# Kernel tuning notes

Hardware: AMD Instinct MI355X
Metric: run time of the kernel (lower is better)

## Reference

```python
import jax, jax.numpy as jnp
import numpy as np

B, M, N, R, FIN, D, H = 16, 512, 512, 8, 4, 256, 4
DH = D // H
LGAT = 2
TF_RATE, THRESH = 0.9, 2.0
GAT_W, ORG_W, DET_W = 0.5, 0.5, 0.5


def setup_inputs() -> dict:
    key = jax.random.key(0)
    ks = jax.random.split(key, 16)
    g = lambda k, shp, fan: jax.random.normal(k, shp, jnp.float32) / np.sqrt(fan)
    inp = {
        'tracks': jax.random.normal(ks[0], (B, M, R, FIN), jnp.float32),
        'detections': jax.random.normal(ks[1], (B, N, FIN), jnp.float32),
        'tracklet_marks': jax.random.randint(ks[2], (B,), M // 2, M + 1, jnp.int32),
        'detection_marks': jax.random.randint(ks[3], (B,), N // 2, N + 1, jnp.int32),
        'feat_W1': g(ks[4], (FIN, D), FIN),
        'feat_b1': jnp.zeros((D,), jnp.float32),
        'feat_W2': g(ks[5], (D, D), D),
        'feat_b2': jnp.zeros((D,), jnp.float32),
        'enc_Wqkv': g(ks[6], (D, 3 * D), D),
        'enc_Wo': g(ks[7], (D, D), D),
        'enc_ff1': g(ks[8], (D, 4 * D), D),
        'enc_ff2': g(ks[9], (4 * D, D), 4 * D),
        'gat_W': g(ks[10], (LGAT, D, D), D),
        'gat_a': g(ks[11], (LGAT, 2, H, DH), DH),
        'det_gat_W': g(ks[12], (LGAT, D, D), D),
        'det_gat_a': g(ks[13], (LGAT, 2, H, DH), DH),
        'cls_Wq': g(ks[14], (2, D, D), D),
        'cls_Wk': g(ks[15], (2, D, D), D),
    }
    return inp


def _ln(x):
    m = jnp.mean(x, -1, keepdims=True)
    v = jnp.var(x, -1, keepdims=True)
    return (x - m) * jax.lax.rsqrt(v + 1e-5)


def _feat(x, W1, b1, W2, b2):
    return jax.nn.elu(x @ W1 + b1) @ W2 + b2


def _encoder(x, Wqkv, Wo, ff1, ff2):
    # x: [T, R, D] -> one pre-LN transformer layer over the rewind axis
    T = x.shape[0]
    h = _ln(x)
    qkv = (h @ Wqkv).reshape(T, R, 3, H, DH)
    q, k, v = qkv[:, :, 0], qkv[:, :, 1], qkv[:, :, 2]
    att = jax.nn.softmax(jnp.einsum('trhd,tshd->thrs', q, k) / np.sqrt(DH), axis=-1)
    o = jnp.einsum('thrs,tshd->trhd', att, v).reshape(T, R, D) @ Wo
    x = x + o
    return x + jax.nn.relu(_ln(x) @ ff1) @ ff2


def _gat(x, adj, W, a):
    # x: [B, Nn, D]; adj: [B, Nn, Nn] bool; a: [2, H, DH]
    b, nn_, _ = x.shape
    h = (x @ W).reshape(b, nn_, H, DH)
    src = jnp.einsum('bnhd,hd->bnh', h, a[0])
    dst = jnp.einsum('bnhd,hd->bnh', h, a[1])
    e = jax.nn.leaky_relu(src[:, :, None, :] + dst[:, None, :, :], 0.2)  # [B,Nn,Nn,H]
    e = jnp.where(adj[..., None], e, -1e9)
    alpha = jax.nn.softmax(e, axis=2)
    out = jnp.einsum('bijh,bjhd->bihd', alpha, h).reshape(b, nn_, D)
    return jax.nn.elu(out)


def _scores(x, adj_f, Wq, Wk):
    s = jax.nn.sigmoid(jnp.einsum('bid,bjd->bij', x @ Wq, x @ Wk) / np.sqrt(D))
    return s * adj_f


def _forward(tracks, detections, tracklet_marks, detection_marks,
             feat_W1, feat_b1, feat_W2, feat_b2,
             enc_Wqkv, enc_Wo, enc_ff1, enc_ff2,
             gat_W, gat_a, det_gat_W, det_gat_a, cls_Wq, cls_Wk):
    tr_emb = _feat(tracks, feat_W1, feat_b1, feat_W2, feat_b2)      # [B,M,R,D]
    det_emb = _feat(detections, feat_W1, feat_b1, feat_W2, feat_b2)  # [B,N,D]

    enc = _encoder(tr_emb.reshape(B * M, R, D), enc_Wqkv, enc_Wo, enc_ff1, enc_ff2)
    enc = enc.reshape(B, M, R, D)
    predicted = tr_emb[:, :, 0, :] + TF_RATE * enc[:, :, 0, :]       # [B,M,D]

    tmask = jnp.arange(M)[None, :] < tracklet_marks[:, None]
    dmask = jnp.arange(N)[None, :] < detection_marks[:, None]

    pos = jnp.concatenate([tracks[:, :, 0, :2], detections[:, :, :2]], axis=1)  # [B,M+N,2]
    vmask = jnp.concatenate([tmask, dmask], axis=1)
    dist = jnp.linalg.norm(pos[:, :, None, :] - pos[:, None, :, :], axis=-1)
    adj = (dist < THRESH) & vmask[:, :, None] & vmask[:, None, :]
    adj_f = adj.astype(jnp.float32)

    feat0 = jnp.concatenate([predicted, det_emb], axis=1)  # [B,M+N,D]
    x = feat0
    for l in range(LGAT):
        x = GAT_W * _gat(x, adj, gat_W[l], gat_a[l]) + ORG_W * feat0
    scores = _scores(x, adj_f, cls_Wq[0], cls_Wk[0])       # [B,M+N,M+N]
    asso_results = scores[:, :M, M:]                        # track->det block

    pd = detections[:, :, :2]
    dist_d = jnp.linalg.norm(pd[:, :, None, :] - pd[:, None, :, :], axis=-1)
    adj_d = (dist_d < THRESH) & dmask[:, :, None] & dmask[:, None, :]
    adj_d_f = adj_d.astype(jnp.float32)

    xd = det_emb
    for l in range(LGAT):
        xd = DET_W * _gat(xd, adj_d, det_gat_W[l], det_gat_a[l]) + ORG_W * det_emb
    det_scores = _scores(xd, adj_d_f, cls_Wq[1], cls_Wk[1])
    det_scores = det_scores * (1.0 - jnp.eye(N, dtype=jnp.float32))  # zero_diag

    return scores, det_scores, asso_results


def reference(tracks, detections, tracklet_marks, detection_marks,
              feat_W1, feat_b1, feat_W2, feat_b2,
              enc_Wqkv, enc_Wo, enc_ff1, enc_ff2,
              gat_W, gat_a, det_gat_W, det_gat_a, cls_Wq, cls_Wk):
    return _forward(tracks, detections, tracklet_marks, detection_marks,
                    feat_W1, feat_b1, feat_W2, feat_b2,
                    enc_Wqkv, enc_Wo, enc_ff1, enc_ff2,
                    gat_W, gat_a, det_gat_W, det_gat_a, cls_Wq, cls_Wk)
```

## Files before the change

kernel.cpp:

```cpp
#include <hip/hip_runtime.h>
#include <math.h>


typedef __bf16 bf16;
typedef __bf16 bf16x8 __attribute__((ext_vector_type(8)));
typedef __bf16 bf16x4 __attribute__((ext_vector_type(4)));
typedef float f32x4 __attribute__((ext_vector_type(4)));

__device__ __forceinline__ float bf2f(bf16 x) { return (float)x; }
__device__ __forceinline__ bf16 f2bf(float x) { return (bf16)x; }

__device__ __forceinline__ bool node_adj(float4 a, float4 c) {
    float dx = a.x - c.x, dy = a.y - c.y;
    return (sqrtf(dx * dx + dy * dy) + a.z + c.z) < 2.0f;
}

struct PrepEnt { const float* src; long dofs; int R; int C; int tstart; };
struct PrepTab { PrepEnt e[13]; };

__global__ __launch_bounds__(256) void k_prep(PrepTab tab, bf16* __restrict__ dst)
{
    __shared__ float tile[32][33];
    const int tid = blockIdx.x;
    int k = 0;
    #pragma unroll
    for (int q = 1; q < 13; ++q) if (tid >= tab.e[q].tstart) k = q;
    PrepEnt E = tab.e[k];
    const int local = tid - E.tstart;
    const int cT = E.C >> 5;
    const int tr = local / cT, tc = local - tr * cT;
    const int r0 = tr << 5, c0 = tc << 5;
    const int t = threadIdx.x;
    {
        int r = t >> 3, cq = (t & 7) * 4;
        *(float4*)&tile[r][cq] = *(const float4*)(E.src + (long)(r0 + r) * E.C + c0 + cq);
    }
    __syncthreads();
    {
        int c = t >> 3, rq = (t & 7) * 4;
        bf16x4 o;
        o[0] = f2bf(tile[rq + 0][c]); o[1] = f2bf(tile[rq + 1][c]);
        o[2] = f2bf(tile[rq + 2][c]); o[3] = f2bf(tile[rq + 3][c]);
        *(bf16x4*)(dst + E.dofs + (long)(c0 + c) * E.R + r0 + rq) = o;
    }
}

__device__ __forceinline__ void gemm_bt(const bf16* __restrict__ A, int lda,
                                        const bf16* __restrict__ BT, int ldb,
                                        int K, f32x4 acc[4])
{
    __shared__ bf16 As[64][40];
    __shared__ bf16 Bs[64][40];
    const int t = threadIdx.x;
    const int m0 = blockIdx.y * 64;
    const int n0 = blockIdx.x * 64;
    const int lane = t & 63, wv = t >> 6, lr = lane & 15, kq = lane >> 4;
    const int arow = t >> 2, acol = (t & 3) * 8;
    for (int k0 = 0; k0 < K; k0 += 32) {
        __syncthreads();
        *(uint4*)&As[arow][acol] = *(const uint4*)(A + (long)(m0 + arow) * lda + k0 + acol);
        *(uint4*)&Bs[arow][acol] = *(const uint4*)(BT + (long)(n0 + arow) * ldb + k0 + acol);
        __syncthreads();
        bf16x8 af = *(const bf16x8*)&As[wv * 16 + lr][kq * 8];
        #pragma unroll
        for (int nt = 0; nt < 4; ++nt) {
            bf16x8 bfr = *(const bf16x8*)&Bs[nt * 16 + lr][kq * 8];
            acc[nt] = __builtin_amdgcn_mfma_f32_16x16x32_bf16(af, bfr, acc[nt], 0, 0, 0);
        }
    }
}

__global__ __launch_bounds__(256) void k_gemm_bf16(
    const bf16* __restrict__ A, int lda,
    const bf16* __restrict__ BT, int ldb,
    bf16* __restrict__ out, int ldo, int K, int relu)
{
    f32x4 acc[4] = {};
    gemm_bt(A, lda, BT, ldb, K, acc);
    const int lane = threadIdx.x & 63, wv = threadIdx.x >> 6;
    const int lr = lane & 15, kq = lane >> 4;
    const int m0 = blockIdx.y * 64, n0 = blockIdx.x * 64;
    #pragma unroll
    for (int nt = 0; nt < 4; ++nt) {
        int col = n0 + nt * 16 + lr;
        #pragma unroll
        for (int i = 0; i < 4; ++i) {
            int row = m0 + wv * 16 + kq * 4 + i;
            float v = acc[nt][i];
            if (relu) v = fmaxf(v, 0.f);
            out[(long)row * ldo + col] = f2bf(v);
        }
    }
}

__global__ __launch_bounds__(256) void k_gemm_addres(
    const bf16* __restrict__ A, int lda,
    const bf16* __restrict__ BT, int ldb,
    const float* __restrict__ res1, int ldr1,
    float* __restrict__ outf, int ldo, int K)
{
    f32x4 acc[4] = {};
    gemm_bt(A, lda, BT, ldb, K, acc);
    const int lane = threadIdx.x & 63, wv = threadIdx.x >> 6;
    const int lr = lane & 15, kq = lane >> 4;
    const int m0 = blockIdx.y * 64, n0 = blockIdx.x * 64;
    #pragma unroll
    for (int nt = 0; nt < 4; ++nt) {
        int col = n0 + nt * 16 + lr;
        #pragma unroll
        for (int i = 0; i < 4; ++i) {
            int row = m0 + wv * 16 + kq * 4 + i;
            outf[(long)row * ldo + col] = res1[(long)row * ldr1 + col] + acc[nt][i];
        }
    }
}

__global__ __launch_bounds__(256) void k_gemm_pred(
    const bf16* __restrict__ A, int lda,
    const bf16* __restrict__ BT, int ldb,
    const float* __restrict__ res1, const float* __restrict__ res2,
    float* __restrict__ outf, bf16* __restrict__ outb, int K)
{
    f32x4 acc[4] = {};
    gemm_bt(A, lda, BT, ldb, K, acc);
    const int lane = threadIdx.x & 63, wv = threadIdx.x >> 6;
    const int lr = lane & 15, kq = lane >> 4;
    const int m0 = blockIdx.y * 64, n0 = blockIdx.x * 64;
    #pragma unroll
    for (int nt = 0; nt < 4; ++nt) {
        int col = n0 + nt * 16 + lr;
        #pragma unroll
        for (int i = 0; i < 4; ++i) {
            int row = m0 + wv * 16 + kq * 4 + i;
            float v = res1[(long)row * 256 + col]
                    + 0.9f * (res2[(long)row * 256 + col] + acc[nt][i]);
            long drow = (long)row + ((row >> 9) << 9);
            long o = drow * 256 + col;
            outf[o] = v;
            outb[o] = f2bf(v);
        }
    }
}

__global__ __launch_bounds__(256) void k_gemm_logits(
    const bf16* __restrict__ A, long sAz,
    const bf16* __restrict__ Bm, long sBz, int K,
    float* __restrict__ out, int ldo, long sOz,
    const float4* __restrict__ nodes, int nodeOfs,
    float* __restrict__ asso, int flags)
{
    f32x4 acc[4] = {};
    const int z = blockIdx.z;
    gemm_bt(A + z * sAz, 256, Bm + z * sBz, 256, K, acc);
    const int lane = threadIdx.x & 63, wv = threadIdx.x >> 6;
    const int lr = lane & 15, kq = lane >> 4;
    const int m0 = blockIdx.y * 64, n0 = blockIdx.x * 64;
    const float4* nb = nodes + z * 1024 + nodeOfs;
    float4 nrow[4], ncol[4];
    #pragma unroll
    for (int i = 0; i < 4; ++i) nrow[i] = nb[m0 + wv * 16 + kq * 4 + i];
    #pragma unroll
    for (int nt = 0; nt < 4; ++nt) ncol[nt] = nb[n0 + nt * 16 + lr];
    float* ob = out + z * sOz;
    #pragma unroll
    for (int nt = 0; nt < 4; ++nt) {
        int col = n0 + nt * 16 + lr;
        #pragma unroll
        for (int i = 0; i < 4; ++i) {
            int row = m0 + wv * 16 + kq * 4 + i;
            bool adj = node_adj(nrow[i], ncol[nt]);
            if ((flags & 2) && row == col) adj = false;
            float v = 0.f;
            if (adj) v = 1.f / (1.f + __expf(-acc[nt][i] * 0.0625f));
            ob[(long)row * ldo + col] = v;
            if ((flags & 1) && row < 512 && col >= 512)
                asso[(long)z * 262144 + (long)row * 512 + (col - 512)] = v;
        }
    }
}

__global__ __launch_bounds__(256) void k_gemm_T(
    const bf16* __restrict__ WT, const bf16* __restrict__ X,
    bf16* __restrict__ hgT, int nN, int nLog)
{
    f32x4 acc[4] = {};
    gemm_bt(WT, 256, X, 256, 256, acc);
    const int lane = threadIdx.x & 63, wv = threadIdx.x >> 6;
    const int lr = lane & 15, kq = lane >> 4;
    const int d0 = blockIdx.y * 64, n0 = blockIdx.x * 64;
    #pragma unroll
    for (int nt = 0; nt < 4; ++nt) {
        int node = n0 + nt * 16 + lr;
        int b = node >> nLog;
        int j = node & (nN - 1);
        #pragma unroll
        for (int i = 0; i < 4; ++i) {
            int d = d0 + wv * 16 + kq * 4 + i;
            hgT[((long)(b * 256 + d) << nLog) + j] = f2bf(acc[nt][i]);
        }
    }
}

__global__ __launch_bounds__(256) void k_featgemm(
    const float* __restrict__ tracks, const float* __restrict__ dets,
    const float* __restrict__ W1, const float* __restrict__ b1,
    const bf16* __restrict__ W2T, const float* __restrict__ b2,
    bf16* __restrict__ emb_b, float* __restrict__ emb_r0_f,
    float* __restrict__ feat0_f, bf16* __restrict__ feat0_b,
    bf16* __restrict__ demb_b)
{
    __shared__ float xr[64][4];
    __shared__ float w1s[4][256];
    __shared__ float b1s[256];
    __shared__ bf16 As[64][40];
    __shared__ bf16 Bs[256][40];
    const int t = threadIdx.x;
    const int m0 = blockIdx.x * 64;
    if (t < 64) {
        int gr = m0 + t;
        const float* sp = (gr < 65536) ? (tracks + (long)gr * 4)
                                       : (dets + (long)(gr - 65536) * 4);
        *(float4*)&xr[t][0] = *(const float4*)sp;
    }
    w1s[0][t] = W1[t];       w1s[1][t] = W1[256 + t];
    w1s[2][t] = W1[512 + t]; w1s[3][t] = W1[768 + t];
    b1s[t] = b1[t];
    const int arow = t >> 2, acol = (t & 3) * 8;
    const int lane = t & 63, wv = t >> 6, lr = lane & 15, kq = lane >> 4;
    f32x4 acc[16] = {};
    __syncthreads();
    for (int k0 = 0; k0 < 256; k0 += 32) {
        __syncthreads();
        #pragma unroll
        for (int j = 0; j < 8; ++j) {
            int c = k0 + acol + j;
            float v = fmaf(xr[arow][0], w1s[0][c],
                      fmaf(xr[arow][1], w1s[1][c],
                      fmaf(xr[arow][2], w1s[2][c],
                      fmaf(xr[arow][3], w1s[3][c], b1s[c]))));
            v = v > 0.f ? v : (__expf(v) - 1.f);
            As[arow][acol + j] = f2bf(v);
        }
        #pragma unroll
        for (int rr = 0; rr < 4; ++rr) {
            int n = rr * 64 + (t >> 2);
            *(uint4*)&Bs[n][acol] = *(const uint4*)(W2T + (long)n * 256 + k0 + acol);
        }
        __syncthreads();
        bf16x8 af = *(const bf16x8*)&As[wv * 16 + lr][kq * 8];
        #pragma unroll
        for (int nt = 0; nt < 16; ++nt) {
            bf16x8 bfr = *(const bf16x8*)&Bs[nt * 16 + lr][kq * 8];
            acc[nt] = __builtin_amdgcn_mfma_f32_16x16x32_bf16(af, bfr, acc[nt], 0, 0, 0);
        }
    }
    #pragma unroll
    for (int nt = 0; nt < 16; ++nt) {
        int col = nt * 16 + lr;
        float bv = b2[col];
        #pragma unroll
        for (int i = 0; i < 4; ++i) {
            int gr = m0 + wv * 16 + kq * 4 + i;
            float v = acc[nt][i] + bv;
            emb_b[(long)gr * 256 + col] = f2bf(v);
            if (gr < 65536) {
                if ((gr & 7) == 0) emb_r0_f[(long)(gr >> 3) * 256 + col] = v;
            } else {
                int dr = gr - 65536;
                long drow = ((long)(dr >> 9) << 10) + 512 + (dr & 511);
                feat0_f[drow * 256 + col] = v;
                feat0_b[drow * 256 + col] = f2bf(v);
                demb_b[(long)dr * 256 + col] = f2bf(v);
            }
        }
    }
}

__global__ __launch_bounds__(256) void k_adjmask(
    const float4* __restrict__ nodes, unsigned long long* __restrict__ adjm,
    int nN, int nLog, int nodeOfs)
{
    const int bi = blockIdx.x;
    const int b = bi >> nLog;
    const int i = bi & (nN - 1);
    const float4* nb = nodes + b * 1024 + nodeOfs;
    const float4 ni = nb[i];
    const int t = threadIdx.x;
    const int w = t >> 6, lane = t & 63;
    const int nC = nN >> 6;
    for (int it = 0; it * 256 < nN; ++it) {
        int j = it * 256 + t;
        bool adj = node_adj(ni, nb[j]);
        unsigned long long mask = __ballot(adj);
        if (lane == 0) adjm[(long)bi * nC + it * 4 + w] = mask;
    }
}

__global__ __launch_bounds__(256) void k_ln_bf16(const bf16* __restrict__ x, bf16* __restrict__ out)
{
    const int w = threadIdx.x >> 6, l = threadIdx.x & 63;
    const long row = (long)blockIdx.x * 4 + w;
    bf16x4 xv = *(const bf16x4*)(x + row * 256 + l * 4);
    float v0 = bf2f(xv[0]), v1 = bf2f(xv[1]), v2 = bf2f(xv[2]), v3 = bf2f(xv[3]);
    float s = v0 + v1 + v2 + v3;
    #pragma unroll
    for (int o = 32; o; o >>= 1) s += __shfl_xor(s, o, 64);
    float mean = s * (1.f / 256.f);
    float d0 = v0 - mean, d1 = v1 - mean, d2 = v2 - mean, d3 = v3 - mean;
    float q = d0 * d0 + d1 * d1 + d2 * d2 + d3 * d3;
    #pragma unroll
    for (int o = 32; o; o >>= 1) q += __shfl_xor(q, o, 64);
    float rstd = rsqrtf(q * (1.f / 256.f) + 1e-5f);
    bf16x4 ov;
    ov[0] = f2bf(d0 * rstd); ov[1] = f2bf(d1 * rstd);
    ov[2] = f2bf(d2 * rstd); ov[3] = f2bf(d3 * rstd);
    *(bf16x4*)(out + row * 256 + l * 4) = ov;
}

__global__ __launch_bounds__(256) void k_ln_f32(const float* __restrict__ x, bf16* __restrict__ out)
{
    const int w = threadIdx.x >> 6, l = threadIdx.x & 63;
    const long row = (long)blockIdx.x * 4 + w;
    float4 xv = *(const float4*)(x + row * 256 + l * 4);
    float s = xv.x + xv.y + xv.z + xv.w;
    #pragma unroll
    for (int o = 32; o; o >>= 1) s += __shfl_xor(s, o, 64);
    float mean = s * (1.f / 256.f);
    float d0 = xv.x - mean, d1 = xv.y - mean, d2 = xv.z - mean, d3 = xv.w - mean;
    float q = d0 * d0 + d1 * d1 + d2 * d2 + d3 * d3;
    #pragma unroll
    for (int o = 32; o; o >>= 1) q += __shfl_xor(q, o, 64);
    float rstd = rsqrtf(q * (1.f / 256.f) + 1e-5f);
    bf16x4 ov;
    ov[0] = f2bf(d0 * rstd); ov[1] = f2bf(d1 * rstd);
    ov[2] = f2bf(d2 * rstd); ov[3] = f2bf(d3 * rstd);
    *(bf16x4*)(out + row * 256 + l * 4) = ov;
}

__global__ __launch_bounds__(256) void k_attn(
    const bf16* __restrict__ q, const bf16* __restrict__ kv,
    bf16* __restrict__ o0)
{
    const long t = blockIdx.x;
    const int h = threadIdx.x >> 6;
    const int lane = threadIdx.x & 63;
    const int s = lane >> 3;
    const int dg = lane & 7;
    const bf16* qp = q + t * 256 + h * 64 + dg * 8;
    const bf16* kp = kv + (t * 8 + s) * 512 + h * 64 + dg * 8;
    float p = 0.f;
    #pragma unroll
    for (int e = 0; e < 8; ++e) p += bf2f(qp[e]) * bf2f(kp[e]);
    p += __shfl_xor(p, 1, 64);
    p += __shfl_xor(p, 2, 64);
    p += __shfl_xor(p, 4, 64);
    float sc = p * 0.125f;
    float w[8];
    float mx = -1e30f;
    #pragma unroll
    for (int s2 = 0; s2 < 8; ++s2) { w[s2] = __shfl(sc, s2 * 8, 64); mx = fmaxf(mx, w[s2]); }
    float sum = 0.f;
    #pragma unroll
    for (int s2 = 0; s2 < 8; ++s2) { w[s2] = __expf(w[s2] - mx); sum += w[s2]; }
    float rs = 1.f / sum;
    float acc = 0.f;
    const bf16* vp = kv + (t * 8) * 512 + 256 + h * 64 + lane;
    #pragma unroll
    for (int s2 = 0; s2 < 8; ++s2) acc += w[s2] * bf2f(vp[(long)s2 * 512]);
    o0[t * 256 + h * 64 + lane] = f2bf(acc * rs);
}

__global__ __launch_bounds__(256) void k_nodes(
    const float* __restrict__ tracks, const float* __restrict__ dets,
    const int* __restrict__ tm, const int* __restrict__ dm,
    float4* __restrict__ nodes)
{
    int idx = blockIdx.x * 256 + threadIdx.x;
    int b = idx >> 10;
    int i = idx & 1023;
    float x, y;
    int valid;
    if (i < 512) {
        long o = (long)(b * 512 + i) * 32;
        x = tracks[o]; y = tracks[o + 1];
        valid = (i < tm[b]) ? 1 : 0;
    } else {
        int n = i - 512;
        long o = (long)(b * 512 + n) * 4;
        x = dets[o]; y = dets[o + 1];
        valid = (n < dm[b]) ? 1 : 0;
    }
    nodes[idx] = make_float4(x, y, valid ? 0.f : 1e9f, 0.f);
}

__global__ __launch_bounds__(256) void k_srcdst_T(
    const bf16* __restrict__ hgT, const float* __restrict__ av,
    float* __restrict__ src, float* __restrict__ dst, int nN, int nLog)
{
    __shared__ float avs[512];
    const int t = threadIdx.x;
    avs[t] = av[t]; avs[256 + t] = av[256 + t];
    __syncthreads();
    const int jl = t & 63, h = t >> 6;
    const int n = blockIdx.x * 64 + jl;
    const int b = n >> nLog, j = n & (nN - 1);
    const bf16* base = hgT + (((long)b * 256 + h * 64) << nLog) + j;
    float p0 = 0.f, p1 = 0.f;
    #pragma unroll 8
    for (int dd = 0; dd < 64; ++dd) {
        float v = bf2f(base[(long)dd << nLog]);
        p0 += v * avs[h * 64 + dd];
        p1 += v * avs[256 + h * 64 + dd];
    }
    src[(long)n * 4 + h] = p0;
    dst[(long)n * 4 + h] = p1;
}

__global__ __launch_bounds__(256) void k_maxdst(
    const float4* __restrict__ dstv, float4* __restrict__ maxd, int nN)
{
    const int b = blockIdx.x;
    const int t = threadIdx.x;
    float4 mv = make_float4(-1e30f, -1e30f, -1e30f, -1e30f);
    for (int j = t; j < nN; j += 256) {
        float4 dj = dstv[(long)b * nN + j];
        mv.x = fmaxf(mv.x, dj.x); mv.y = fmaxf(mv.y, dj.y);
        mv.z = fmaxf(mv.z, dj.z); mv.w = fmaxf(mv.w, dj.w);
    }
    __shared__ float4 red[256];
    red[t] = mv;
    __syncthreads();
    for (int off = 128; off; off >>= 1) {
        if (t < off) {
            float4 a = red[t], c = red[t + off];
            red[t] = make_float4(fmaxf(a.x, c.x), fmaxf(a.y, c.y),
                                 fmaxf(a.z, c.z), fmaxf(a.w, c.w));
        }
        __syncthreads();
    }
    if (t == 0) maxd[b] = red[0];
}

__global__ __launch_bounds__(256) void k_gatagg_mm(
    const bf16* __restrict__ hgT,
    const unsigned long long* __restrict__ adjm,
    const float4* __restrict__ srcv, const float4* __restrict__ maxd,
    const float4* __restrict__ dstv,
    const float* __restrict__ res, int resBatchStride,
    bf16* __restrict__ outb, int nN)
{
    __shared__ float dstT[4][1024];
    __shared__ unsigned int adjW[32][33];
    const int t = threadIdx.x;
    const int nblk = nN >> 5;
    const int b = blockIdx.x / nblk;
    const int i0 = (blockIdx.x - b * nblk) << 5;
    const int nC = nN >> 6;
    for (int j = t; j < nN; j += 256) {
        float4 dj = dstv[(long)b * nN + j];
        dstT[0][j] = dj.x; dstT[1][j] = dj.y; dstT[2][j] = dj.z; dstT[3][j] = dj.w;
    }
    for (int idx = t; idx < 32 * nC; idx += 256) {
        int r = idx / nC, c = idx - r * nC;
        unsigned long long v = adjm[((long)b * nN + i0 + r) * nC + c];
        adjW[r][c * 2] = (unsigned)v;
        adjW[r][c * 2 + 1] = (unsigned)(v >> 32);
    }
    __syncthreads();
    const int h = t >> 6, lane = t & 63, lr = lane & 15, kq = lane >> 4;
    const float mdh = ((const float*)(maxd + b))[h];
    float s_r[2], m_r[2], psum[2] = {0.f, 0.f};
    #pragma unroll
    for (int mt = 0; mt < 2; ++mt) {
        long idx = (long)b * nN + i0 + mt * 16 + lr;
        s_r[mt] = ((const float*)(srcv + idx))[h];
        float tmp = s_r[mt] + mdh;
        m_r[mt] = fmaxf(tmp, 0.2f * tmp);
    }
    f32x4 acc[2][4] = {};
    const bf16* hb = hgT + ((long)b * 256 + h * 64) * nN;
    for (int j0 = 0; j0 < nN; j0 += 32) {
        bf16x8 bfr[4];
        #pragma unroll
        for (int nt = 0; nt < 4; ++nt)
            bfr[nt] = *(const bf16x8*)(hb + (long)(nt * 16 + lr) * nN + j0 + kq * 8);
        #pragma unroll
        for (int mt = 0; mt < 2; ++mt) {
            unsigned byte = (adjW[mt * 16 + lr][j0 >> 5] >> (kq * 8)) & 0xffu;
            bf16x8 af;
            float ps = 0.f;
            #pragma unroll
            for (int jj = 0; jj < 8; ++jj) {
                float e = s_r[mt] + dstT[h][j0 + kq * 8 + jj];
                e = fmaxf(e, 0.2f * e);
                e = (byte & (1u << jj)) ? e : -1e9f;
                float p = __expf(e - m_r[mt]);
                af[jj] = f2bf(p);
                ps += p;
            }
            psum[mt] += ps;
            #pragma unroll
            for (int nt = 0; nt < 4; ++nt)
                acc[mt][nt] = __builtin_amdgcn_mfma_f32_16x16x32_bf16(af, bfr[nt], acc[mt][nt], 0, 0, 0);
        }
    }
    float stot[2];
    #pragma unroll
    for (int mt = 0; mt < 2; ++mt) {
        float v = psum[mt];
        v += __shfl_xor(v, 16, 64);
        v += __shfl_xor(v, 32, 64);
        stot[mt] = v;
    }
    #pragma unroll
    for (int mt = 0; mt < 2; ++mt) {
        #pragma unroll
        for (int ii = 0; ii < 4; ++ii) {
            int i = i0 + mt * 16 + kq * 4 + ii;
            long bi = (long)b * nN + i;
            float sv = __shfl(stot[mt], kq * 4 + ii, 64);
            float rs = 1.f / fmaxf(sv, 1e-30f);
            #pragma unroll
            for (int nt = 0; nt < 4; ++nt) {
                int col = h * 64 + nt * 16 + lr;
                float a = acc[mt][nt][ii] * rs;
                float e = a > 0.f ? a : expm1f(a);
                float v = 0.5f * e + 0.5f * res[(long)b * resBatchStride + (long)i * 256 + col];
                outb[bi * 256 + col] = f2bf(v);
            }
        }
    }
}

extern "C" void kernel_launch(void* const* d_in, const int* in_sizes, int n_in,
                              void* d_out, int out_size, void* d_ws, size_t ws_size,
                              hipStream_t stream)
{
    (void)in_sizes; (void)n_in; (void)out_size; (void)ws_size;
    const float* tracks = (const float*)d_in[0];
    const float* dets   = (const float*)d_in[1];
    const int*  tmarks = (const int*)d_in[2];
    const int*  dmarks = (const int*)d_in[3];
    const float* W1   = (const float*)d_in[4];
    const float* b1   = (const float*)d_in[5];
    const float* W2   = (const float*)d_in[6];
    const float* b2   = (const float*)d_in[7];
    const float* Wqkv = (const float*)d_in[8];
    const float* Wo   = (const float*)d_in[9];
    const float* eff1 = (const float*)d_in[10];
    const float* eff2 = (const float*)d_in[11];
    const float* gatW = (const float*)d_in[12];
    const float* gatA = (const float*)d_in[13];
    const float* dgatW = (const float*)d_in[14];
    const float* dgatA = (const float*)d_in[15];
    const float* clsWq = (const float*)d_in[16];
    const float* clsWk = (const float*)d_in[17];
    float* out = (float*)d_out;

    char* wsb = (char*)d_ws;
    size_t off = 0;
    auto take = [&](size_t bytes) -> char* {
        char* p = wsb + off;
        off += (bytes + 255) & ~(size_t)255;
        return p;
    };
    char* R_emb  = take(37748736);
    char* R_r0   = take(8388608);
    char* R_hln  = take(33554432);
    char* R_v    = take(33554432);
    char* R_gat  = take(25165824);
    char* R_q    = take(4194304);
    char* R_o0   = take(4194304);
    char* R_f0f  = take(16777216);
    char* R_f0b  = take(8388608);
    char* R_demb = take(4194304);
    float4* nodes = (float4*)take(262144);
    float4* src4  = (float4*)take(262144);
    float4* dst4  = (float4*)take(262144);
    float4* maxd4 = (float4*)take(256);
    unsigned long long* adjm_main = (unsigned long long*)take(2097152);
    unsigned long long* adjm_det  = (unsigned long long*)take(524288);
    bf16* wbuf = (bf16*)take(2752512);

    bf16*  emb_b    = (bf16*)R_emb;
    float* emb_r0_f = (float*)R_r0;
    bf16*  hln      = (bf16*)R_hln;
    bf16*  kv_b     = (bf16*)d_out;
    bf16*  q_b      = (bf16*)R_q;
    bf16*  o0_b     = (bf16*)R_o0;
    float* x20      = (float*)R_emb;
    bf16*  h2_b     = (bf16*)(R_emb + 8388608);
    bf16*  f1_b     = (bf16*)R_hln;
    float* feat0_f  = (float*)R_f0f;
    bf16*  feat0_b  = (bf16*)R_f0b;
    bf16*  demb_b   = (bf16*)R_demb;
    bf16*  hgT      = (bf16*)R_gat;
    bf16*  xga_b    = (bf16*)(R_gat + 8388608);
    bf16*  xgb_b    = (bf16*)(R_gat + 16777216);
    bf16*  xq_b     = (bf16*)R_v;
    bf16*  xk_b     = (bf16*)(R_v + 8388608);

    bf16* W2T    = wbuf + 0;
    bf16* WqkvT  = wbuf + 65536;
    bf16* WoT    = wbuf + 262144;
    bf16* eff1T  = wbuf + 327680;
    bf16* eff2T  = wbuf + 589824;
    bf16* gatW0T = wbuf + 851968;
    bf16* gatW1T = wbuf + 917504;
    bf16* dgatW0T= wbuf + 983040;
    bf16* dgatW1T= wbuf + 1048576;
    bf16* clsWq0T= wbuf + 1114112;
    bf16* clsWk0T= wbuf + 1179648;
    bf16* clsWq1T= wbuf + 1245184;
    bf16* clsWk1T= wbuf + 1310720;
    PrepTab tab;
    tab.e[0]  = { W2,             0,       256,  256,  0    };
    tab.e[1]  = { Wqkv,           65536,   256,  768,  64   };
    tab.e[2]  = { Wo,             262144,  256,  256,  256  };
    tab.e[3]  = { eff1,           327680,  256,  1024, 320  };
    tab.e[4]  = { eff2,           589824,  1024, 256,  576  };
    tab.e[5]  = { gatW,           851968,  256,  256,  832  };
    tab.e[6]  = { gatW + 65536,   917504,  256,  256,  896  };
    tab.e[7]  = { dgatW,          983040,  256,  256,  960  };
    tab.e[8]  = { dgatW + 65536,  1048576, 256,  256,  1024 };
    tab.e[9]  = { clsWq,          1114112, 256,  256,  1088 };
    tab.e[10] = { clsWk,          1179648, 256,  256,  1152 };
    tab.e[11] = { clsWq + 65536,  1245184, 256,  256,  1216 };
    tab.e[12] = { clsWk + 65536,  1310720, 256,  256,  1280 };

    k_prep<<<1344, 256, 0, stream>>>(tab, wbuf);
    k_nodes<<<64, 256, 0, stream>>>(tracks, dets, tmarks, dmarks, nodes);
    k_adjmask<<<16384, 256, 0, stream>>>(nodes, adjm_main, 1024, 10, 0);
    k_adjmask<<<8192, 256, 0, stream>>>(nodes, adjm_det, 512, 9, 512);
    k_featgemm<<<1152, 256, 0, stream>>>(tracks, dets, W1, b1, W2T, b2,
        emb_b, emb_r0_f, feat0_f, feat0_b, demb_b);

    k_ln_bf16<<<16384, 256, 0, stream>>>(emb_b, hln);
    k_gemm_bf16<<<dim3(8, 1024, 1), 256, 0, stream>>>(hln, 256, WqkvT + 65536, 256, kv_b, 512, 256, 0);
    k_gemm_bf16<<<dim3(4, 128, 1), 256, 0, stream>>>(hln, 2048, WqkvT, 256, q_b, 256, 256, 0);
    k_attn<<<8192, 256, 0, stream>>>(q_b, kv_b, o0_b);
    k_gemm_addres<<<dim3(4, 128, 1), 256, 0, stream>>>(o0_b, 256, WoT, 256, emb_r0_f, 256, x20, 256, 256);
    k_ln_f32<<<2048, 256, 0, stream>>>(x20, h2_b);
    k_gemm_bf16<<<dim3(16, 128, 1), 256, 0, stream>>>(h2_b, 256, eff1T, 256, f1_b, 1024, 256, 1);
    k_gemm_pred<<<dim3(4, 128, 1), 256, 0, stream>>>(f1_b, 1024, eff2T, 1024, emb_r0_f, x20, feat0_f, feat0_b, 1024);

    k_gemm_T<<<dim3(256, 4, 1), 256, 0, stream>>>(gatW0T, feat0_b, hgT, 1024, 10);
    k_srcdst_T<<<256, 256, 0, stream>>>(hgT, gatA, (float*)src4, (float*)dst4, 1024, 10);
    k_maxdst<<<16, 256, 0, stream>>>(dst4, maxd4, 1024);
    k_gatagg_mm<<<512, 256, 0, stream>>>(hgT, adjm_main, src4, maxd4, dst4,
        feat0_f, 262144, xga_b, 1024);
    k_gemm_T<<<dim3(256, 4, 1), 256, 0, stream>>>(gatW1T, xga_b, hgT, 1024, 10);
    k_srcdst_T<<<256, 256, 0, stream>>>(hgT, gatA + 512, (float*)src4, (float*)dst4, 1024, 10);
    k_maxdst<<<16, 256, 0, stream>>>(dst4, maxd4, 1024);
    k_gatagg_mm<<<512, 256, 0, stream>>>(hgT, adjm_main, src4, maxd4, dst4,
        feat0_f, 262144, xgb_b, 1024);
    k_gemm_bf16<<<dim3(4, 256, 1), 256, 0, stream>>>(xgb_b, 256, clsWq0T, 256, xq_b, 256, 256, 0);
    k_gemm_bf16<<<dim3(4, 256, 1), 256, 0, stream>>>(xgb_b, 256, clsWk0T, 256, xk_b, 256, 256, 0);
    k_gemm_logits<<<dim3(16, 16, 16), 256, 0, stream>>>(xq_b, 262144L, xk_b, 262144L, 256,
        out, 1024, 1048576L, nodes, 0, out + 20971520L, 1);

    k_gemm_T<<<dim3(128, 4, 1), 256, 0, stream>>>(dgatW0T, demb_b, hgT, 512, 9);
    k_srcdst_T<<<128, 256, 0, stream>>>(hgT, dgatA, (float*)src4, (float*)dst4, 512, 9);
    k_maxdst<<<16, 256, 0, stream>>>(dst4, maxd4, 512);
    k_gatagg_mm<<<256, 256, 0, stream>>>(hgT, adjm_det, src4, maxd4, dst4,
        feat0_f + 131072, 262144, xga_b, 512);
    k_gemm_T<<<dim3(128, 4, 1), 256, 0, stream>>>(dgatW1T, xga_b, hgT, 512, 9);
    k_srcdst_T<<<128, 256, 0, stream>>>(hgT, dgatA + 512, (float*)src4, (float*)dst4, 512, 9);
    k_maxdst<<<16, 256, 0, stream>>>(dst4, maxd4, 512);
    k_gatagg_mm<<<256, 256, 0, stream>>>(hgT, adjm_det, src4, maxd4, dst4,
        feat0_f + 131072, 262144, xgb_b, 512);
    k_gemm_bf16<<<dim3(4, 128, 1), 256, 0, stream>>>(xgb_b, 256, clsWq1T, 256, xq_b, 256, 256, 0);
    k_gemm_bf16<<<dim3(4, 128, 1), 256, 0, stream>>>(xgb_b, 256, clsWk1T, 256, xk_b, 256, 256, 0);
    k_gemm_logits<<<dim3(8, 8, 16), 256, 0, stream>>>(xq_b, 131072L, xk_b, 131072L, 256,
        out + 16777216L, 512, 262144L, nodes, 512, (float*)nullptr, 2);
}
```

Baseline: 601.0 us.

## Use 128x128 GEMM tiles, fuse Q/K projections, atomic max-dst, merged adjmask launch

Adds a 128x128-tile MFMA GEMM core and uses it for the KV projection, FF1, and the score logits. The logits now take adjacency from the precomputed bitmask instead of recomputing distances. The classifier Q and K projections are merged into one GEMM writing interleaved [Q|K] rows, and the two adjmask launches are merged into one. The separate max-dst reduction kernel is replaced by a wave reduction plus an atomicMax on order-preserving encoded floats inside srcdst, with initialisation done in k_nodes. Together these cut launches and global traffic, and raise reuse per tile. The cost is larger tiles that may lower occupancy, and dependence on Q and K weights being contiguous in the weight buffer.

```diff
diff --git a/kernel.cpp b/kernel.cpp
--- a/kernel.cpp
+++ b/kernel.cpp
@@ -9,6 +9,15 @@
 
 __device__ __forceinline__ float bf2f(bf16 x) { return (float)x; }
 __device__ __forceinline__ bf16 f2bf(float x) { return (bf16)x; }
+
+__device__ __forceinline__ unsigned encf(float f) {
+    unsigned u = __float_as_uint(f);
+    return (u & 0x80000000u) ? ~u : (u | 0x80000000u);
+}
+__device__ __forceinline__ float decf(unsigned u) {
+    return (u & 0x80000000u) ? __uint_as_float(u & 0x7fffffffu)
+                             : __uint_as_float(~u);
+}
 
 __device__ __forceinline__ bool node_adj(float4 a, float4 c) {
     float dx = a.x - c.x, dy = a.y - c.y;
@@ -70,6 +79,100 @@
     }
 }
 
+__device__ __forceinline__ void gemm128_core(const bf16* __restrict__ A, int lda,
+                                             const bf16* __restrict__ BT, int ldb,
+                                             int m0, int n0, int K, f32x4 acc[2][8])
+{
+    __shared__ bf16 As[128][40];
+    __shared__ bf16 Bs[128][40];
+    const int t = threadIdx.x;
+    const int lane = t & 63, wv = t >> 6, lr = lane & 15, kq = lane >> 4;
+    const int srow = t >> 1, scol = (t & 1) * 16;
+    for (int k0 = 0; k0 < K; k0 += 32) {
+        __syncthreads();
+        {
+            const bf16* ap = A + (long)(m0 + srow) * lda + k0 + scol;
+            *(uint4*)&As[srow][scol] = *(const uint4*)ap;
+            *(uint4*)&As[srow][scol + 8] = *(const uint4*)(ap + 8);
+            const bf16* bp = BT + (long)(n0 + srow) * ldb + k0 + scol;
+            *(uint4*)&Bs[srow][scol] = *(const uint4*)bp;
+            *(uint4*)&Bs[srow][scol + 8] = *(const uint4*)(bp + 8);
+        }
+        __syncthreads();
+        bf16x8 af[2];
+        af[0] = *(const bf16x8*)&As[wv * 32 + lr][kq * 8];
+        af[1] = *(const bf16x8*)&As[wv * 32 + 16 + lr][kq * 8];
+        #pragma unroll
+        for (int nt = 0; nt < 8; ++nt) {
+            bf16x8 bfr = *(const bf16x8*)&Bs[nt * 16 + lr][kq * 8];
+            acc[0][nt] = __builtin_amdgcn_mfma_f32_16x16x32_bf16(af[0], bfr, acc[0][nt], 0, 0, 0);
+            acc[1][nt] = __builtin_amdgcn_mfma_f32_16x16x32_bf16(af[1], bfr, acc[1][nt], 0, 0, 0);
+        }
+    }
+}
+
+__global__ __launch_bounds__(256) void k_gemm128_bf16(
+    const bf16* __restrict__ A, int lda,
+    const bf16* __restrict__ BT, int ldb,
+    bf16* __restrict__ out, int ldo, int K, int relu)
+{
+    f32x4 acc[2][8] = {};
+    const int m0 = blockIdx.y * 128, n0 = blockIdx.x * 128;
+    gemm128_core(A, lda, BT, ldb, m0, n0, K, acc);
+    const int lane = threadIdx.x & 63, wv = threadIdx.x >> 6;
+    const int lr = lane & 15, kq = lane >> 4;
+    #pragma unroll
+    for (int mt = 0; mt < 2; ++mt) {
+        #pragma unroll
+        for (int nt = 0; nt < 8; ++nt) {
+            int col = n0 + nt * 16 + lr;
+            #pragma unroll
+            for (int i = 0; i < 4; ++i) {
+                int row = m0 + wv * 32 + mt * 16 + kq * 4 + i;
+                float v = acc[mt][nt][i];
+                if (relu) v = fmaxf(v, 0.f);
+                out[(long)row * ldo + col] = f2bf(v);
+            }
+        }
+    }
+}
+
+__global__ __launch_bounds__(256) void k_gemm128_logits(
+    const bf16* __restrict__ xqk, long sAz, int K,
+    float* __restrict__ out, int ldo, long sOz,
+    const unsigned long long* __restrict__ adjm, int nN, int nC,
+    float* __restrict__ asso, int flags)
+{
+    f32x4 acc[2][8] = {};
+    const int z = blockIdx.z;
+    const int m0 = blockIdx.y * 128, n0 = blockIdx.x * 128;
+    gemm128_core(xqk + z * sAz, 512, xqk + z * sAz + 256, 512, m0, n0, K, acc);
+    const int lane = threadIdx.x & 63, wv = threadIdx.x >> 6;
+    const int lr = lane & 15, kq = lane >> 4;
+    float* ob = out + z * sOz;
+    #pragma unroll
+    for (int mt = 0; mt < 2; ++mt) {
+        #pragma unroll
+        for (int i = 0; i < 4; ++i) {
+            int row = m0 + wv * 32 + mt * 16 + kq * 4 + i;
+            unsigned long long w0 = adjm[((long)z * nN + row) * nC + (n0 >> 6)];
+            unsigned long long w1 = adjm[((long)z * nN + row) * nC + (n0 >> 6) + 1];
+            #pragma unroll
+            for (int nt = 0; nt < 8; ++nt) {
+                int col = n0 + nt * 16 + lr;
+                int bp = nt * 16 + lr;
+                bool adj = (bp < 64) ? ((w0 >> bp) & 1ull) : ((w1 >> (bp - 64)) & 1ull);
+                if ((flags & 2) && row == col) adj = false;
+                float v = 0.f;
+                if (adj) v = 1.f / (1.f + __expf(-acc[mt][nt][i] * 0.0625f));
+                ob[(long)row * ldo + col] = v;
+                if ((flags & 1) && row < 512 && col >= 512)
+                    asso[(long)z * 262144 + (long)row * 512 + (col - 512)] = v;
+            }
+        }
+    }
+}
+
 __global__ __launch_bounds__(256) void k_gemm_bf16(
     const bf16* __restrict__ A, int lda,
     const bf16* __restrict__ BT, int ldb,
@@ -138,43 +241,6 @@
             long o = drow * 256 + col;
             outf[o] = v;
             outb[o] = f2bf(v);
-        }
-    }
-}
-
-__global__ __launch_bounds__(256) void k_gemm_logits(
-    const bf16* __restrict__ A, long sAz,
-    const bf16* __restrict__ Bm, long sBz, int K,
-    float* __restrict__ out, int ldo, long sOz,
-    const float4* __restrict__ nodes, int nodeOfs,
-    float* __restrict__ asso, int flags)
-{
-    f32x4 acc[4] = {};
-    const int z = blockIdx.z;
-    gemm_bt(A + z * sAz, 256, Bm + z * sBz, 256, K, acc);
-    const int lane = threadIdx.x & 63, wv = threadIdx.x >> 6;
-    const int lr = lane & 15, kq = lane >> 4;
-    const int m0 = blockIdx.y * 64, n0 = blockIdx.x * 64;
-    const float4* nb = nodes + z * 1024 + nodeOfs;
-    float4 nrow[4], ncol[4];
-    #pragma unroll
-    for (int i = 0; i < 4; ++i) nrow[i] = nb[m0 + wv * 16 + kq * 4 + i];
-    #pragma unroll
-    for (int nt = 0; nt < 4; ++nt) ncol[nt] = nb[n0 + nt * 16 + lr];
-    float* ob = out + z * sOz;
-    #pragma unroll
-    for (int nt = 0; nt < 4; ++nt) {
-        int col = n0 + nt * 16 + lr;
-        #pragma unroll
-        for (int i = 0; i < 4; ++i) {
-            int row = m0 + wv * 16 + kq * 4 + i;
-            bool adj = node_adj(nrow[i], ncol[nt]);
-            if ((flags & 2) && row == col) adj = false;
-            float v = 0.f;
-            if (adj) v = 1.f / (1.f + __expf(-acc[nt][i] * 0.0625f));
-            ob[(long)row * ldo + col] = v;
-            if ((flags & 1) && row < 512 && col >= 512)
-                asso[(long)z * 262144 + (long)row * 512 + (col - 512)] = v;
         }
     }
 }
@@ -277,10 +343,14 @@
 }
 
 __global__ __launch_bounds__(256) void k_adjmask(
-    const float4* __restrict__ nodes, unsigned long long* __restrict__ adjm,
-    int nN, int nLog, int nodeOfs)
-{
-    const int bi = blockIdx.x;
+    const float4* __restrict__ nodes,
+    unsigned long long* __restrict__ adjm_main,
+    unsigned long long* __restrict__ adjm_det)
+{
+    int bi, nN, nLog, nodeOfs;
+    unsigned long long* adjm;
+    if (blockIdx.x < 16384) { bi = blockIdx.x; nN = 1024; nLog = 10; nodeOfs = 0; adjm = adjm_main; }
+    else { bi = blockIdx.x - 16384; nN = 512; nLog = 9; nodeOfs = 512; adjm = adjm_det; }
     const int b = bi >> nLog;
     const int i = bi & (nN - 1);
     const float4* nb = nodes + b * 1024 + nodeOfs;
@@ -373,9 +443,10 @@
 __global__ __launch_bounds__(256) void k_nodes(
     const float* __restrict__ tracks, const float* __restrict__ dets,
     const int* __restrict__ tm, const int* __restrict__ dm,
-    float4* __restrict__ nodes)
+    float4* __restrict__ nodes, unsigned* __restrict__ maxd_all)
 {
     int idx = blockIdx.x * 256 + threadIdx.x;
+    if (blockIdx.x == 0) maxd_all[threadIdx.x] = 0x007fffffu;
     int b = idx >> 10;
     int i = idx & 1023;
     float x, y;
@@ -395,7 +466,8 @@
 
 __global__ __launch_bounds__(256) void k_srcdst_T(
     const bf16* __restrict__ hgT, const float* __restrict__ av,
-    float* __restrict__ src, float* __restrict__ dst, int nN, int nLog)
+    float* __restrict__ src, float* __restrict__ dst,
+    unsigned* __restrict__ maxd_enc, int nN, int nLog)
 {
     __shared__ float avs[512];
     const int t = threadIdx.x;
@@ -414,37 +486,16 @@
     }
     src[(long)n * 4 + h] = p0;
     dst[(long)n * 4 + h] = p1;
-}
-
-__global__ __launch_bounds__(256) void k_maxdst(
-    const float4* __restrict__ dstv, float4* __restrict__ maxd, int nN)
-{
-    const int b = blockIdx.x;
-    const int t = threadIdx.x;
-    float4 mv = make_float4(-1e30f, -1e30f, -1e30f, -1e30f);
-    for (int j = t; j < nN; j += 256) {
-        float4 dj = dstv[(long)b * nN + j];
-        mv.x = fmaxf(mv.x, dj.x); mv.y = fmaxf(mv.y, dj.y);
-        mv.z = fmaxf(mv.z, dj.z); mv.w = fmaxf(mv.w, dj.w);
-    }
-    __shared__ float4 red[256];
-    red[t] = mv;
-    __syncthreads();
-    for (int off = 128; off; off >>= 1) {
-        if (t < off) {
-            float4 a = red[t], c = red[t + off];
-            red[t] = make_float4(fmaxf(a.x, c.x), fmaxf(a.y, c.y),
-                                 fmaxf(a.z, c.z), fmaxf(a.w, c.w));
-        }
-        __syncthreads();
-    }
-    if (t == 0) maxd[b] = red[0];
+    float m = p1;
+    #pragma unroll
+    for (int o = 32; o; o >>= 1) m = fmaxf(m, __shfl_xor(m, o, 64));
+    if (jl == 0) atomicMax(&maxd_enc[b * 4 + h], encf(m));
 }
 
 __global__ __launch_bounds__(256) void k_gatagg_mm(
     const bf16* __restrict__ hgT,
     const unsigned long long* __restrict__ adjm,
-    const float4* __restrict__ srcv, const float4* __restrict__ maxd,
+    const float4* __restrict__ srcv, const unsigned* __restrict__ maxd_enc,
     const float4* __restrict__ dstv,
     const float* __restrict__ res, int resBatchStride,
     bf16* __restrict__ outb, int nN)
@@ -468,7 +519,7 @@
     }
     __syncthreads();
     const int h = t >> 6, lane = t & 63, lr = lane & 15, kq = lane >> 4;
-    const float mdh = ((const float*)(maxd + b))[h];
+    const float mdh = decf(maxd_enc[b * 4 + h]);
     float s_r[2], m_r[2], psum[2] = {0.f, 0.f};
     #pragma unroll
     for (int mt = 0; mt < 2; ++mt) {
@@ -577,7 +628,7 @@
     float4* nodes = (float4*)take(262144);
     float4* src4  = (float4*)take(262144);
     float4* dst4  = (float4*)take(262144);
-    float4* maxd4 = (float4*)take(256);
+    unsigned* maxd_all = (unsigned*)take(1024);
     unsigned long long* adjm_main = (unsigned long long*)take(2097152);
     unsigned long long* adjm_det  = (unsigned long long*)take(524288);
     bf16* wbuf = (bf16*)take(2752512);
@@ -597,8 +648,7 @@
     bf16*  hgT      = (bf16*)R_gat;
     bf16*  xga_b    = (bf16*)(R_gat + 8388608);
     bf16*  xgb_b    = (bf16*)(R_gat + 16777216);
-    bf16*  xq_b     = (bf16*)R_v;
-    bf16*  xk_b     = (bf16*)(R_v + 8388608);
+    bf16*  xqk_b    = (bf16*)R_v;
 
     bf16* W2T    = wbuf + 0;
     bf16* WqkvT  = wbuf + 65536;
@@ -609,10 +659,8 @@
     bf16* gatW1T = wbuf + 917504;
     bf16* dgatW0T= wbuf + 983040;
     bf16* dgatW1T= wbuf + 1048576;
-    bf16* clsWq0T= wbuf + 1114112;
-    bf16* clsWk0T= wbuf + 1179648;
-    bf16* clsWq1T= wbuf + 1245184;
-    bf16* clsWk1T= wbuf + 1310720;
+    bf16* clsQK0T= wbuf + 1114112;
+    bf16* clsQK1T= wbuf + 1245184;
     PrepTab tab;
     tab.e[0]  = { W2,             0,       256,  256,  0    };
     tab.e[1]  = { Wqkv,           65536,   256,  768,  64   };
@@ -629,48 +677,41 @@
     tab.e[12] = { clsWk + 65536,  1310720, 256,  256,  1280 };
 
     k_prep<<<1344, 256, 0, stream>>>(tab, wbuf);
-    k_nodes<<<64, 256, 0, stream>>>(tracks, dets, tmarks, dmarks, nodes);
-    k_adjmask<<<16384, 256, 0, stream>>>(nodes, adjm_main, 1024, 10, 0);
-    k_adjmask<<<8192, 256, 0, stream>>>(nodes, adjm_det, 512, 9, 512);
+    k_nodes<<<64, 256, 0, stream>>>(tracks, dets, tmarks, dmarks, nodes, maxd_all);
+    k_adjmask<<<24576, 256, 0, stream>>>(nodes, adjm_main, adjm_det);
     k_featgemm<<<1152, 256, 0, stream>>>(tracks, dets, W1, b1, W2T, b2,
         emb_b, emb_r0_f, feat0_f, feat0_b, demb_b);
 
     k_ln_bf16<<<16384, 256, 0, stream>>>(emb_b, hln);
-    k_gemm_bf16<<<dim3(8, 1024, 1), 256, 0, stream>>>(hln, 256, WqkvT + 65536, 256, kv_b, 512, 256, 0);
+    k_gemm128_bf16<<<dim3(4, 512, 1), 256, 0, stream>>>(hln, 256, WqkvT + 65536, 256, kv_b, 512, 256, 0);
     k_gemm_bf16<<<dim3(4, 128, 1), 256, 0, stream>>>(hln, 2048, WqkvT, 256, q_b, 256, 256, 0);
     k_attn<<<8192, 256, 0, stream>>>(q_b, kv_b, o0_b);
     k_gemm_addres<<<dim3(4, 128, 1), 256, 0, stream>>>(o0_b, 256, WoT, 256, emb_r0_f, 256, x20, 256, 256);
     k_ln_f32<<<2048, 256, 0, stream>>>(x20, h2_b);
-    k_gemm_bf16<<<dim3(16, 128, 1), 256, 0, stream>>>(h2_b, 256, eff1T, 256, f1_b, 1024, 256, 1);
+    k_gemm128_bf16<<<dim3(8, 64, 1), 256, 0, stream>>>(h2_b, 256, eff1T, 256, f1_b, 1024, 256, 1);
     k_gemm_pred<<<dim3(4, 128, 1), 256, 0, stream>>>(f1_b, 1024, eff2T, 1024, emb_r0_f, x20, feat0_f, feat0_b, 1024);
 
     k_gemm_T<<<dim3(256, 4, 1), 256, 0, stream>>>(gatW0T, feat0_b, hgT, 1024, 10);
-    k_srcdst_T<<<256, 256, 0, stream>>>(hgT, gatA, (float*)src4, (float*)dst4, 1024, 10);
-    k_maxdst<<<16, 256, 0, stream>>>(dst4, maxd4, 1024);
-    k_gatagg_mm<<<512, 256, 0, stream>>>(hgT, adjm_main, src4, maxd4, dst4,
+    k_srcdst_T<<<256, 256, 0, stream>>>(hgT, gatA, (float*)src4, (float*)dst4, maxd_all, 1024, 10);
+    k_gatagg_mm<<<512, 256, 0, stream>>>(hgT, adjm_main, src4, maxd_all, dst4,
         feat0_f, 262144, xga_b, 1024);
     k_gemm_T<<<dim3(256, 4, 1), 256, 0, stream>>>(gatW1T, xga_b, hgT, 1024, 10);
-    k_srcdst_T<<<256, 256, 0, stream>>>(hgT, gatA + 512, (float*)src4, (float*)dst4, 1024, 10);
-    k_maxdst<<<16, 256, 0, stream>>>(dst4, maxd4, 1024);
-    k_gatagg_mm<<<512, 256, 0, stream>>>(hgT, adjm_main, src4, maxd4, dst4,
+    k_srcdst_T<<<256, 256, 0, stream>>>(hgT, gatA + 512, (float*)src4, (float*)dst4, maxd_all + 64, 1024, 10);
+    k_gatagg_mm<<<512, 256, 0, stream>>>(hgT, adjm_main, src4, maxd_all + 64, dst4,
         feat0_f, 262144, xgb_b, 1024);
-    k_gemm_bf16<<<dim3(4, 256, 1), 256, 0, stream>>>(xgb_b, 256, clsWq0T, 256, xq_b, 256, 256, 0);
-    k_gemm_bf16<<<dim3(4, 256, 1), 256, 0, stream>>>(xgb_b, 256, clsWk0T, 256, xk_b, 256, 256, 0);
-    k_gemm_logits<<<dim3(16, 16, 16), 256, 0, stream>>>(xq_b, 262144L, xk_b, 262144L, 256,
-        out, 1024, 1048576L, nodes, 0, out + 20971520L, 1);
+    k_gemm_bf16<<<dim3(8, 256, 1), 256, 0, stream>>>(xgb_b, 256, clsQK0T, 256, xqk_b, 512, 256, 0);
+    k_gemm128_logits<<<dim3(8, 8, 16), 256, 0, stream>>>(xqk_b, 524288L, 256,
+        out, 1024, 1048576L, adjm_main, 1024, 16, out + 20971520L, 1);
 
     k_gemm_T<<<dim3(128, 4, 1), 256, 0, stream>>>(dgatW0T, demb_b, hgT, 512, 9);
-    k_srcdst_T<<<128, 256, 0, stream>>>(hgT, dgatA, (float*)src4, (float*)dst4, 512, 9);
-    k_maxdst<<<16, 256, 0, stream>>>(dst4, maxd4, 512);
-    k_gatagg_mm<<<256, 256, 0, stream>>>(hgT, adjm_det, src4, maxd4, dst4,
+    k_srcdst_T<<<128, 256, 0, stream>>>(hgT, dgatA, (float*)src4, (float*)dst4, maxd_all + 128, 512, 9);
+    k_gatagg_mm<<<256, 256, 0, stream>>>(hgT, adjm_det, src4, maxd_all + 128, dst4,
         feat0_f + 131072, 262144, xga_b, 512);
     k_gemm_T<<<dim3(128, 4, 1), 256, 0, stream>>>(dgatW1T, xga_b, hgT, 512, 9);
-    k_srcdst_T<<<128, 256, 0, stream>>>(hgT, dgatA + 512, (float*)src4, (float*)dst4, 512, 9);
-    k_maxdst<<<16, 256, 0, stream>>>(dst4, maxd4, 512);
-    k_gatagg_mm<<<256, 256, 0, stream>>>(hgT, adjm_det, src4, maxd4, dst4,
+    k_srcdst_T<<<128, 256, 0, stream>>>(hgT, dgatA + 512, (float*)src4, (float*)dst4, maxd_all + 192, 512, 9);
+    k_gatagg_mm<<<256, 256, 0, stream>>>(hgT, adjm_det, src4, maxd_all + 192, dst4,
         feat0_f + 131072, 262144, xgb_b, 512);
-    k_gemm_bf16<<<dim3(4, 128, 1), 256, 0, stream>>>(xgb_b, 256, clsWq1T, 256, xq_b, 256, 256, 0);
-    k_gemm_bf16<<<dim3(4, 128, 1), 256, 0, stream>>>(xgb_b, 256, clsWk1T, 256, xk_b, 256, 256, 0);
-    k_gemm_logits<<<dim3(8, 8, 16), 256, 0, stream>>>(xq_b, 131072L, xk_b, 131072L, 256,
-        out + 16777216L, 512, 262144L, nodes, 512, (float*)nullptr, 2);
-}
+    k_gemm_bf16<<<dim3(8, 128, 1), 256, 0, stream>>>(xgb_b, 256, clsQK1T, 256, xqk_b, 512, 256, 0);
+    k_gemm128_logits<<<dim3(4, 4, 16), 256, 0, stream>>>(xqk_b, 262144L, 256,
+        out + 16777216L, 512, 262144L, adjm_det, 512, 8, (float*)nullptr, 2);
+}
```

New measurement: 590.3 us. No clear change (-1.8%).
